# Kernel optimization log

Hardware: AMD Instinct MI355X
Metric: run time of the kernel (lower is better)

## Reference

```python
import jax, jax.numpy as jnp
import numpy as np

B, S, H = 32, 2048, 1024

def setup_inputs() -> dict:
    key = jax.random.key(0)
    ks = jax.random.split(key, 8)
    s = 1.0 / np.sqrt(H)
    return {
        "query": jax.random.normal(ks[0], (B, 1, H), jnp.float32),
        "keys": jax.random.normal(ks[1], (B, S, H), jnp.float32),
        "Wa_w": jax.random.normal(ks[2], (H, H), jnp.float32) * s,
        "Wa_b": jax.random.normal(ks[3], (H,), jnp.float32) * s,
        "Ua_w": jax.random.normal(ks[4], (H, H), jnp.float32) * s,
        "Ua_b": jax.random.normal(ks[5], (H,), jnp.float32) * s,
        "Va_w": jax.random.normal(ks[6], (1, H), jnp.float32) * s,
        "Va_b": jax.random.normal(ks[7], (1,), jnp.float32) * s,
    }

def reference(query, keys, Wa_w, Wa_b, Ua_w, Ua_b, Va_w, Va_b):
    # Wa(query): (B,1,H); Ua(keys): (B,S,H); broadcast add -> (B,S,H)
    q = jnp.einsum('bqh,oh->bqo', query, Wa_w) + Wa_b
    k = jnp.einsum('bsh,oh->bso', keys, Ua_w) + Ua_b
    h = jnp.tanh(q + k)                              # (B,S,H)
    scores = jnp.einsum('bsh,oh->bso', h, Va_w) + Va_b  # (B,S,1)
    scores = scores[:, :, 0][:, None, :]             # (B,1,S)
    weights = jax.nn.softmax(scores, axis=-1)        # (B,1,S)
    context = jnp.einsum('bqs,bsh->bqh', weights, keys)  # (B,1,H)
    return context, weights
```

## Files before the change

kernel.cpp:

```cpp
#include <hip/hip_runtime.h>
#include <hip/hip_bf16.h>

#define HDIM 1024
#define SEQ  2048
#define BATCH 32
#define M_TOTAL (BATCH * SEQ)

typedef __bf16 bf16x8 __attribute__((ext_vector_type(8)));
typedef float  f32x4  __attribute__((ext_vector_type(4)));
typedef unsigned short u16;

__device__ __forceinline__ u16 f2bf(float f) {
    unsigned int u = __float_as_uint(f);
    u += 0x7FFFu + ((u >> 16) & 1u);
    return (u16)(u >> 16);
}

__global__ __launch_bounds__(256) void cvt_kernel(const float* __restrict__ in,
                                                  u16* __restrict__ out) {
    size_t i = ((size_t)blockIdx.x * 256 + threadIdx.x) * 8;
    float4 f0 = *(const float4*)(in + i);
    float4 f1 = *(const float4*)(in + i + 4);
    uint4 v;
    v.x = (unsigned)f2bf(f0.x) | ((unsigned)f2bf(f0.y) << 16);
    v.y = (unsigned)f2bf(f0.z) | ((unsigned)f2bf(f0.w) << 16);
    v.z = (unsigned)f2bf(f1.x) | ((unsigned)f2bf(f1.y) << 16);
    v.w = (unsigned)f2bf(f1.z) | ((unsigned)f2bf(f1.w) << 16);
    *(uint4*)(out + i) = v;
}

__global__ __launch_bounds__(256) void qb_kernel(const float* __restrict__ query,
                                                 const float* __restrict__ Wa_w,
                                                 const float* __restrict__ Wa_b,
                                                 const float* __restrict__ Ua_b,
                                                 float* __restrict__ qb) {
    __shared__ float qs[HDIM];
    const int b = blockIdx.x;
    const int tid = threadIdx.x;
    ((float4*)qs)[tid] = ((const float4*)(query + b * HDIM))[tid];
    __syncthreads();
    const int lane = tid & 63;
    const int w = tid >> 6;
    const int obase = blockIdx.y * 64 + w * 16;
    for (int i = 0; i < 16; i++) {
        int o = obase + i;
        const float4* wrow = (const float4*)(Wa_w + (size_t)o * HDIM);
        float s = 0.f;
        #pragma unroll
        for (int j = 0; j < 4; j++) {
            float4 wv = wrow[j * 64 + lane];
            float4 qv = ((const float4*)qs)[j * 64 + lane];
            s += wv.x * qv.x + wv.y * qv.y + wv.z * qv.z + wv.w * qv.w;
        }
        #pragma unroll
        for (int m = 1; m < 64; m <<= 1) s += __shfl_xor(s, m);
        if (lane == 0) qb[b * HDIM + o] = s + Wa_b[o] + Ua_b[o];
    }
}

__global__ __launch_bounds__(256) void gemm_score_kernel(const u16* __restrict__ keysb,
                                                         const u16* __restrict__ uab,
                                                         const float* __restrict__ qb,
                                                         const float* __restrict__ vaw,
                                                         float* __restrict__ scores) {
    __shared__ __align__(16) u16 As[128 * 32];
    __shared__ __align__(16) u16 Bs[128 * 32];
    const int tid  = threadIdx.x;
    const int lane = tid & 63;
    const int w    = tid >> 6;
    const int n0 = blockIdx.x * 128;
    const int m0 = blockIdx.y * 128;
    const int wave_m = (w & 1) * 64;
    const int wave_n = (w >> 1) * 64;

    f32x4 acc[4][4] = {};

    const int srow = w * 32 + (lane >> 2);
    const int scol = (lane & 3) * 8;
    const u16* gA = keysb + (size_t)(m0 + srow) * HDIM + scol;
    const u16* gB = uab   + (size_t)(n0 + srow) * HDIM + scol;
    u16* lA0 = As + w * 32 * 32;
    u16* lA1 = As + (w * 32 + 16) * 32;
    u16* lB0 = Bs + w * 32 * 32;
    u16* lB1 = Bs + (w * 32 + 16) * 32;

    const int fr = lane & 15;
    const int fq = lane >> 4;

    for (int k0 = 0; k0 < HDIM; k0 += 32) {
        __syncthreads();
        __builtin_amdgcn_global_load_lds((__attribute__((address_space(1))) void*)(gA + k0),
                                         (__attribute__((address_space(3))) void*)lA0, 16, 0, 0);
        __builtin_amdgcn_global_load_lds((__attribute__((address_space(1))) void*)(gA + k0 + 16 * HDIM),
                                         (__attribute__((address_space(3))) void*)lA1, 16, 0, 0);
        __builtin_amdgcn_global_load_lds((__attribute__((address_space(1))) void*)(gB + k0),
                                         (__attribute__((address_space(3))) void*)lB0, 16, 0, 0);
        __builtin_amdgcn_global_load_lds((__attribute__((address_space(1))) void*)(gB + k0 + 16 * HDIM),
                                         (__attribute__((address_space(3))) void*)lB1, 16, 0, 0);
        __syncthreads();

        bf16x8 a[4], b[4];
        #pragma unroll
        for (int i = 0; i < 4; i++) {
            a[i] = *(const bf16x8*)(As + (wave_m + i * 16 + fr) * 32 + fq * 8);
            b[i] = *(const bf16x8*)(Bs + (wave_n + i * 16 + fr) * 32 + fq * 8);
        }
        #pragma unroll
        for (int mi = 0; mi < 4; mi++)
            #pragma unroll
            for (int ni = 0; ni < 4; ni++)
                acc[mi][ni] = __builtin_amdgcn_mfma_f32_16x16x32_bf16(a[mi], b[ni], acc[mi][ni], 0, 0, 0);
    }

    const int bidx = m0 >> 11;
    float qv[4], vv[4];
    #pragma unroll
    for (int ni = 0; ni < 4; ni++) {
        int n_g = n0 + wave_n + ni * 16 + fr;
        qv[ni] = qb[bidx * HDIM + n_g];
        vv[ni] = vaw[n_g];
    }
    #pragma unroll
    for (int mi = 0; mi < 4; mi++) {
        #pragma unroll
        for (int r = 0; r < 4; r++) {
            float p = 0.f;
            #pragma unroll
            for (int ni = 0; ni < 4; ni++) {
                float x = acc[mi][ni][r] + qv[ni];
                float e = __expf(2.f * x);
                p += (1.f - 2.f / (e + 1.f)) * vv[ni];
            }
            p += __shfl_xor(p, 1);
            p += __shfl_xor(p, 2);
            p += __shfl_xor(p, 4);
            p += __shfl_xor(p, 8);
            if (fr == 0) {
                int s_g = (m0 + wave_m + mi * 16 + fq * 4 + r) & (SEQ - 1);
                atomicAdd(scores + bidx * SEQ + s_g, p);
            }
        }
    }
}

__global__ __launch_bounds__(256) void softmax_kernel(const float* __restrict__ scores,
                                                      float* __restrict__ weights) {
    __shared__ float red[4];
    const int b = blockIdx.x;
    const int tid = threadIdx.x;
    float v[8];
    float mx = -1e30f;
    #pragma unroll
    for (int i = 0; i < 8; i++) {
        v[i] = scores[b * SEQ + tid + i * 256];
        mx = fmaxf(mx, v[i]);
    }
    #pragma unroll
    for (int m = 1; m < 64; m <<= 1) mx = fmaxf(mx, __shfl_xor(mx, m));
    if ((tid & 63) == 0) red[tid >> 6] = mx;
    __syncthreads();
    mx = fmaxf(fmaxf(red[0], red[1]), fmaxf(red[2], red[3]));
    float sum = 0.f;
    #pragma unroll
    for (int i = 0; i < 8; i++) { v[i] = __expf(v[i] - mx); sum += v[i]; }
    #pragma unroll
    for (int m = 1; m < 64; m <<= 1) sum += __shfl_xor(sum, m);
    __syncthreads();
    if ((tid & 63) == 0) red[tid >> 6] = sum;
    __syncthreads();
    sum = red[0] + red[1] + red[2] + red[3];
    float inv = 1.f / sum;
    #pragma unroll
    for (int i = 0; i < 8; i++) weights[b * SEQ + tid + i * 256] = v[i] * inv;
}

__global__ __launch_bounds__(256) void context_kernel(const float* __restrict__ keys,
                                                      const float* __restrict__ weights,
                                                      float* __restrict__ ctx) {
    __shared__ float wsm[128];
    const int b = blockIdx.x;
    const int s0 = blockIdx.y * 128;
    const int tid = threadIdx.x;
    if (tid < 128) wsm[tid] = weights[b * SEQ + s0 + tid];
    __syncthreads();
    float ax = 0.f, ay = 0.f, az = 0.f, aw = 0.f;
    const float4* kp = (const float4*)(keys + (size_t)b * SEQ * HDIM + (size_t)s0 * HDIM) + tid;
    #pragma unroll 4
    for (int s = 0; s < 128; s++) {
        float4 kv = kp[s * 256];
        float wv = wsm[s];
        ax += wv * kv.x; ay += wv * kv.y; az += wv * kv.z; aw += wv * kv.w;
    }
    float* o = ctx + b * HDIM + tid * 4;
    atomicAdd(o + 0, ax);
    atomicAdd(o + 1, ay);
    atomicAdd(o + 2, az);
    atomicAdd(o + 3, aw);
}

extern "C" void kernel_launch(void* const* d_in, const int* in_sizes, int n_in,
                              void* d_out, int out_size, void* d_ws, size_t ws_size,
                              hipStream_t stream) {
    const float* query = (const float*)d_in[0];
    const float* keys  = (const float*)d_in[1];
    const float* Wa_w  = (const float*)d_in[2];
    const float* Wa_b  = (const float*)d_in[3];
    const float* Ua_w  = (const float*)d_in[4];
    const float* Ua_b  = (const float*)d_in[5];
    const float* Va_w  = (const float*)d_in[6];
    float* out = (float*)d_out;

    char* ws = (char*)d_ws;
    u16*  keysb  = (u16*)ws;
    u16*  uab    = (u16*)(ws + 134217728);
    float* qb    = (float*)(ws + 134217728 + 2097152);
    float* scores= (float*)(ws + 134217728 + 2097152 + 131072);

    hipMemsetAsync(scores, 0, BATCH * SEQ * sizeof(float), stream);
    hipMemsetAsync(out, 0, BATCH * HDIM * sizeof(float), stream);

    cvt_kernel<<<(BATCH * SEQ * HDIM) / 2048, 256, 0, stream>>>(keys, keysb);
    cvt_kernel<<<(HDIM * HDIM) / 2048, 256, 0, stream>>>(Ua_w, uab);
    qb_kernel<<<dim3(BATCH, HDIM / 64), 256, 0, stream>>>(query, Wa_w, Wa_b, Ua_b, qb);
    gemm_score_kernel<<<dim3(HDIM / 128, M_TOTAL / 128), 256, 0, stream>>>(keysb, uab, qb, Va_w, scores);
    softmax_kernel<<<BATCH, 256, 0, stream>>>(scores, out + BATCH * HDIM);
    context_kernel<<<dim3(BATCH, SEQ / 128), 256, 0, stream>>>(keys, out + BATCH * HDIM, out);
}
```

Measured before the change: 667.0 us.

## Enlarge GEMM tile to 256x128, replace score atomics with per-slice partials

The score GEMM tile grows to 256x128, with each wave computing 128x64, so each B tile is reused across more rows. The grid order is swapped so M varies fastest. Score atomics are replaced by plain stores into 16 per-N-slice partial buffers, which the softmax kernel sums. Softmax also zeroes the context output, so both memsets go away. The context kernel is split into finer 64-row chunks. The costs are higher register pressure from 32 accumulators, a larger partial buffer, and more atomics in the context kernel.

```diff
diff --git a/kernel.cpp b/kernel.cpp
--- a/kernel.cpp
+++ b/kernel.cpp
@@ -5,10 +5,16 @@
 #define SEQ  2048
 #define BATCH 32
 #define M_TOTAL (BATCH * SEQ)
+#define BM 256
+#define BN 128
+#define BK 32
+#define NSLICE 16
 
 typedef __bf16 bf16x8 __attribute__((ext_vector_type(8)));
 typedef float  f32x4  __attribute__((ext_vector_type(4)));
 typedef unsigned short u16;
+#define AS1 __attribute__((address_space(1)))
+#define AS3 __attribute__((address_space(3)))
 
 __device__ __forceinline__ u16 f2bf(float f) {
     unsigned int u = __float_as_uint(f);
@@ -58,55 +64,54 @@
     }
 }
 
-__global__ __launch_bounds__(256) void gemm_score_kernel(const u16* __restrict__ keysb,
-                                                         const u16* __restrict__ uab,
-                                                         const float* __restrict__ qb,
-                                                         const float* __restrict__ vaw,
-                                                         float* __restrict__ scores) {
-    __shared__ __align__(16) u16 As[128 * 32];
-    __shared__ __align__(16) u16 Bs[128 * 32];
+__global__ __launch_bounds__(256, 2) void gemm_score_kernel(const u16* __restrict__ keysb,
+                                                            const u16* __restrict__ uab,
+                                                            const float* __restrict__ qb,
+                                                            const float* __restrict__ vaw,
+                                                            float* __restrict__ sp) {
+    __shared__ __align__(16) u16 As[BM * BK];
+    __shared__ __align__(16) u16 Bs[BN * BK];
     const int tid  = threadIdx.x;
     const int lane = tid & 63;
     const int w    = tid >> 6;
-    const int n0 = blockIdx.x * 128;
-    const int m0 = blockIdx.y * 128;
-    const int wave_m = (w & 1) * 64;
+    const int m0 = blockIdx.x * BM;
+    const int n0 = blockIdx.y * BN;
+    const int wave_m = (w & 1) * 128;
     const int wave_n = (w >> 1) * 64;
 
-    f32x4 acc[4][4] = {};
-
-    const int srow = w * 32 + (lane >> 2);
+    f32x4 acc[8][4] = {};
+
+    const int srow = lane >> 2;
     const int scol = (lane & 3) * 8;
-    const u16* gA = keysb + (size_t)(m0 + srow) * HDIM + scol;
-    const u16* gB = uab   + (size_t)(n0 + srow) * HDIM + scol;
-    u16* lA0 = As + w * 32 * 32;
-    u16* lA1 = As + (w * 32 + 16) * 32;
-    u16* lB0 = Bs + w * 32 * 32;
-    u16* lB1 = Bs + (w * 32 + 16) * 32;
+    const u16* gA = keysb + (size_t)(m0 + w * 64 + srow) * HDIM + scol;
+    const u16* gB = uab   + (size_t)(n0 + w * 32 + srow) * HDIM + scol;
+    u16* lA = As + (w * 64) * BK;
+    u16* lB = Bs + (w * 32) * BK;
 
     const int fr = lane & 15;
     const int fq = lane >> 4;
 
-    for (int k0 = 0; k0 < HDIM; k0 += 32) {
+    for (int k0 = 0; k0 < HDIM; k0 += BK) {
         __syncthreads();
-        __builtin_amdgcn_global_load_lds((__attribute__((address_space(1))) void*)(gA + k0),
-                                         (__attribute__((address_space(3))) void*)lA0, 16, 0, 0);
-        __builtin_amdgcn_global_load_lds((__attribute__((address_space(1))) void*)(gA + k0 + 16 * HDIM),
-                                         (__attribute__((address_space(3))) void*)lA1, 16, 0, 0);
-        __builtin_amdgcn_global_load_lds((__attribute__((address_space(1))) void*)(gB + k0),
-                                         (__attribute__((address_space(3))) void*)lB0, 16, 0, 0);
-        __builtin_amdgcn_global_load_lds((__attribute__((address_space(1))) void*)(gB + k0 + 16 * HDIM),
-                                         (__attribute__((address_space(3))) void*)lB1, 16, 0, 0);
+        #pragma unroll
+        for (int i = 0; i < 4; i++)
+            __builtin_amdgcn_global_load_lds((AS1 void*)(gA + k0 + i * 16 * HDIM),
+                                             (AS3 void*)(lA + i * 16 * BK), 16, 0, 0);
+        #pragma unroll
+        for (int i = 0; i < 2; i++)
+            __builtin_amdgcn_global_load_lds((AS1 void*)(gB + k0 + i * 16 * HDIM),
+                                             (AS3 void*)(lB + i * 16 * BK), 16, 0, 0);
         __syncthreads();
 
-        bf16x8 a[4], b[4];
-        #pragma unroll
-        for (int i = 0; i < 4; i++) {
-            a[i] = *(const bf16x8*)(As + (wave_m + i * 16 + fr) * 32 + fq * 8);
-            b[i] = *(const bf16x8*)(Bs + (wave_n + i * 16 + fr) * 32 + fq * 8);
-        }
-        #pragma unroll
-        for (int mi = 0; mi < 4; mi++)
+        bf16x8 a[8], b[4];
+        #pragma unroll
+        for (int i = 0; i < 8; i++)
+            a[i] = *(const bf16x8*)(As + (wave_m + i * 16 + fr) * BK + fq * 8);
+        #pragma unroll
+        for (int i = 0; i < 4; i++)
+            b[i] = *(const bf16x8*)(Bs + (wave_n + i * 16 + fr) * BK + fq * 8);
+        #pragma unroll
+        for (int mi = 0; mi < 8; mi++)
             #pragma unroll
             for (int ni = 0; ni < 4; ni++)
                 acc[mi][ni] = __builtin_amdgcn_mfma_f32_16x16x32_bf16(a[mi], b[ni], acc[mi][ni], 0, 0, 0);
@@ -120,8 +125,10 @@
         qv[ni] = qb[bidx * HDIM + n_g];
         vv[ni] = vaw[n_g];
     }
-    #pragma unroll
-    for (int mi = 0; mi < 4; mi++) {
+    const int slice = blockIdx.y * 2 + (w >> 1);
+    float* sl = sp + ((size_t)slice * BATCH + bidx) * SEQ;
+    #pragma unroll
+    for (int mi = 0; mi < 8; mi++) {
         #pragma unroll
         for (int r = 0; r < 4; r++) {
             float p = 0.f;
@@ -137,23 +144,30 @@
             p += __shfl_xor(p, 8);
             if (fr == 0) {
                 int s_g = (m0 + wave_m + mi * 16 + fq * 4 + r) & (SEQ - 1);
-                atomicAdd(scores + bidx * SEQ + s_g, p);
+                sl[s_g] = p;
             }
         }
     }
 }
 
-__global__ __launch_bounds__(256) void softmax_kernel(const float* __restrict__ scores,
-                                                      float* __restrict__ weights) {
+__global__ __launch_bounds__(256) void softmax_kernel(const float* __restrict__ sp,
+                                                      float* __restrict__ weights,
+                                                      float* __restrict__ ctx) {
     __shared__ float red[4];
     const int b = blockIdx.x;
     const int tid = threadIdx.x;
+    float4 z = {0.f, 0.f, 0.f, 0.f};
+    ((float4*)(ctx + b * HDIM))[tid] = z;
     float v[8];
     float mx = -1e30f;
     #pragma unroll
     for (int i = 0; i < 8; i++) {
-        v[i] = scores[b * SEQ + tid + i * 256];
-        mx = fmaxf(mx, v[i]);
+        int s = tid + i * 256;
+        float a = 0.f;
+        #pragma unroll
+        for (int j = 0; j < NSLICE; j++) a += sp[((size_t)j * BATCH + b) * SEQ + s];
+        v[i] = a;
+        mx = fmaxf(mx, a);
     }
     #pragma unroll
     for (int m = 1; m < 64; m <<= 1) mx = fmaxf(mx, __shfl_xor(mx, m));
@@ -177,16 +191,16 @@
 __global__ __launch_bounds__(256) void context_kernel(const float* __restrict__ keys,
                                                       const float* __restrict__ weights,
                                                       float* __restrict__ ctx) {
-    __shared__ float wsm[128];
+    __shared__ float wsm[64];
     const int b = blockIdx.x;
-    const int s0 = blockIdx.y * 128;
+    const int s0 = blockIdx.y * 64;
     const int tid = threadIdx.x;
-    if (tid < 128) wsm[tid] = weights[b * SEQ + s0 + tid];
+    if (tid < 64) wsm[tid] = weights[b * SEQ + s0 + tid];
     __syncthreads();
     float ax = 0.f, ay = 0.f, az = 0.f, aw = 0.f;
     const float4* kp = (const float4*)(keys + (size_t)b * SEQ * HDIM + (size_t)s0 * HDIM) + tid;
-    #pragma unroll 4
-    for (int s = 0; s < 128; s++) {
+    #pragma unroll 8
+    for (int s = 0; s < 64; s++) {
         float4 kv = kp[s * 256];
         float wv = wsm[s];
         ax += wv * kv.x; ay += wv * kv.y; az += wv * kv.z; aw += wv * kv.w;
@@ -211,18 +225,15 @@
     float* out = (float*)d_out;
 
     char* ws = (char*)d_ws;
-    u16*  keysb  = (u16*)ws;
-    u16*  uab    = (u16*)(ws + 134217728);
-    float* qb    = (float*)(ws + 134217728 + 2097152);
-    float* scores= (float*)(ws + 134217728 + 2097152 + 131072);
-
-    hipMemsetAsync(scores, 0, BATCH * SEQ * sizeof(float), stream);
-    hipMemsetAsync(out, 0, BATCH * HDIM * sizeof(float), stream);
+    u16*  keysb = (u16*)ws;
+    u16*  uab   = (u16*)(ws + 134217728);
+    float* qb   = (float*)(ws + 134217728 + 2097152);
+    float* sp   = (float*)(ws + 134217728 + 2097152 + 131072);
 
     cvt_kernel<<<(BATCH * SEQ * HDIM) / 2048, 256, 0, stream>>>(keys, keysb);
     cvt_kernel<<<(HDIM * HDIM) / 2048, 256, 0, stream>>>(Ua_w, uab);
     qb_kernel<<<dim3(BATCH, HDIM / 64), 256, 0, stream>>>(query, Wa_w, Wa_b, Ua_b, qb);
-    gemm_score_kernel<<<dim3(HDIM / 128, M_TOTAL / 128), 256, 0, stream>>>(keysb, uab, qb, Va_w, scores);
-    softmax_kernel<<<BATCH, 256, 0, stream>>>(scores, out + BATCH * HDIM);
-    context_kernel<<<dim3(BATCH, SEQ / 128), 256, 0, stream>>>(keys, out + BATCH * HDIM, out);
-}
+    gemm_score_kernel<<<dim3(M_TOTAL / BM, HDIM / BN), 256, 0, stream>>>(keysb, uab, qb, Va_w, sp);
+    softmax_kernel<<<BATCH, 256, 0, stream>>>(sp, out + BATCH * HDIM, out);
+    context_kernel<<<dim3(BATCH, SEQ / 64), 256, 0, stream>>>(keys, out + BATCH * HDIM, out);
+}
```

New measurement: 671.9 us. Within noise of the previous version (+0.7%).
